# Performance work log

Hardware: AMD Instinct MI355X
Metric: run time of the kernel (lower is better)

Reference implementation:

```python
import jax, jax.numpy as jnp
import numpy as np

B, T, C, H = 4, 2048, 1024, 64


def setup_inputs() -> dict:
    key = jax.random.key(0)
    kx, kk, kq, kv = jax.random.split(key, 4)
    scale = 1.0 / np.sqrt(C)
    return {
        "x": jax.random.normal(kx, (B, T, C), dtype=jnp.float32),
        "Wk": jax.random.normal(kk, (C, H), dtype=jnp.float32) * scale,
        "Wq": jax.random.normal(kq, (C, H), dtype=jnp.float32) * scale,
        "Wv": jax.random.normal(kv, (C, H), dtype=jnp.float32) * scale,
    }


def reference(x, Wk, Wq, Wv):
    # projections: [B, T, H]
    k = jnp.einsum("btc,ch->bth", x, Wk)
    q = jnp.einsum("btc,ch->bth", x, Wq)
    v = jnp.einsum("btc,ch->bth", x, Wv)
    # attention scores [B, T, T], scaled by sqrt(head_size)
    scores = jnp.einsum("bqh,bkh->bqk", q, k) / jnp.sqrt(jnp.asarray(H, x.dtype))
    # causal mask (decoder)
    causal = jnp.tril(jnp.ones((T, T), dtype=bool))
    scores = jnp.where(causal, scores, -jnp.inf)
    attn = jax.nn.softmax(scores, axis=-1)
    # dropout p=0.0 (eval) -> identity
    return jnp.einsum("bqk,bkh->bqh", attn, v)
```

## Files before the change

### kernel.cpp

```cpp
#include <hip/hip_runtime.h>
#include <hip/hip_bf16.h>

#define BB 4
#define TT 2048
#define CC 1024
#define HH 64
#define LOG2E 1.4426950408889634f

typedef __attribute__((ext_vector_type(8))) unsigned short ushort8;
typedef __attribute__((ext_vector_type(4))) unsigned short ushort4v;
typedef __attribute__((ext_vector_type(8))) __bf16 bf16x8;
typedef __attribute__((ext_vector_type(4))) float float4v;

static __device__ __forceinline__ unsigned short f2bf(float f) {
    return __builtin_bit_cast(unsigned short, (__bf16)f);
}

static __device__ __forceinline__ float4v mfma16(ushort8 a, ushort8 b, float4v c) {
    return __builtin_amdgcn_mfma_f32_16x16x32_bf16(
        __builtin_bit_cast(bf16x8, a), __builtin_bit_cast(bf16x8, b), c, 0, 0, 0);
}

static __device__ __forceinline__ ushort8 cvt8(float4v a, float4v b) {
    ushort8 r;
#pragma unroll
    for (int i = 0; i < 4; ++i) { r[i] = f2bf(a[i]); r[4 + i] = f2bf(b[i]); }
    return r;
}

__global__ __launch_bounds__(256) void wconv_kernel(
    const float* __restrict__ Wq, const float* __restrict__ Wk,
    const float* __restrict__ Wv, unsigned short* __restrict__ wf)
{
    __shared__ __align__(16) float ws[3][64][64];
    const int kc = blockIdx.x;
    const int t = threadIdx.x;
    const int r = t >> 2, c4 = (t & 3) << 4;
    const float* Ws[3] = {Wq, Wk, Wv};
#pragma unroll
    for (int y = 0; y < 3; ++y) {
        const float* src = Ws[y] + (size_t)(kc * 64 + r) * HH + c4;
#pragma unroll
        for (int i = 0; i < 4; ++i)
            *(float4v*)&ws[y][r][c4 + 4 * i] = *(const float4v*)(src + 4 * i);
    }
    __syncthreads();
#pragma unroll
    for (int i = 0; i < 6; ++i) {
        const int U = t + 256 * i;
        const int lane = U & 63, qq = U >> 6;
        const int nt = qq % 12, ks = qq / 12;
        const int y = nt >> 2;
        const int col = 16 * (nt & 3) + (lane & 15);
        const int kl = ks * 32 + 8 * (lane >> 4);
        ushort8 p;
#pragma unroll
        for (int j = 0; j < 8; ++j) p[j] = f2bf(ws[y][kl + j][col]);
        *(ushort8*)&wf[((size_t)kc * 1536 + U) * 8] = p;
    }
}

__global__ __launch_bounds__(768) void proj_kernel(
    const float* __restrict__ x, const unsigned short* __restrict__ wf,
    unsigned short* __restrict__ qo, unsigned short* __restrict__ ko,
    unsigned short* __restrict__ vo)
{
    __shared__ __align__(16) unsigned short xa[2][2048];

    const int t0 = blockIdx.x << 5;
    const int tid = threadIdx.x;
    const int w = tid >> 6;
    const int lane = tid & 63;
    const int l15 = lane & 15, g = lane >> 4;

    ushort8 bw[16][2];
#pragma unroll
    for (int kc = 0; kc < 16; ++kc)
#pragma unroll
        for (int ks = 0; ks < 2; ++ks)
            bw[kc][ks] = *(const ushort8*)
                &wf[(size_t)(((kc * 2 + ks) * 12 + w) * 64 + lane) * 8];

    const int sr = tid >> 3, su = tid & 7;
    const int soff = (sr * 8 + (su ^ (sr & 7))) * 8;
    const float* xp = x + (size_t)(t0 + sr) * CC + su * 8;

    const int sw = l15 & 7;
    const int r00 = (l15 * 8 + (g ^ sw)) * 8;
    const int r01 = (l15 * 8 + ((4 + g) ^ sw)) * 8;
    const int r10 = ((16 + l15) * 8 + (g ^ sw)) * 8;
    const int r11 = ((16 + l15) * 8 + ((4 + g) ^ sw)) * 8;

    float4v ac0 = (float4v)0.0f, ac1 = (float4v)0.0f;

    if (tid < 256)
        *(ushort8*)&xa[0][soff] =
            cvt8(*(const float4v*)xp, *(const float4v*)(xp + 4));
    __syncthreads();

#pragma unroll
    for (int kc = 0; kc < 16; ++kc) {
        const int cur = kc & 1, nxt = cur ^ 1;
        float4v u0, u1;
        if (kc < 15 && tid < 256) {
            u0 = *(const float4v*)(xp + (kc + 1) * 64);
            u1 = *(const float4v*)(xp + (kc + 1) * 64 + 4);
        }
        const unsigned short* xb = xa[cur];
        ushort8 a00 = *(const ushort8*)&xb[r00];
        ushort8 a01 = *(const ushort8*)&xb[r01];
        ushort8 a10 = *(const ushort8*)&xb[r10];
        ushort8 a11 = *(const ushort8*)&xb[r11];
        if (w < 8) {
            ac0 = mfma16(a00, bw[kc][0], ac0);
            ac0 = mfma16(a01, bw[kc][1], ac0);
            ac1 = mfma16(a10, bw[kc][0], ac1);
            ac1 = mfma16(a11, bw[kc][1], ac1);
        } else {
            ac0 = mfma16(bw[kc][0], a00, ac0);
            ac0 = mfma16(bw[kc][1], a01, ac0);
            ac1 = mfma16(bw[kc][0], a10, ac1);
            ac1 = mfma16(bw[kc][1], a11, ac1);
        }
        if (kc < 15 && tid < 256)
            *(ushort8*)&xa[nxt][soff] = cvt8(u0, u1);
        __syncthreads();
    }

    if (w < 8) {
        const float sc = (w < 4) ? 0.125f * LOG2E : 1.0f;
        unsigned short* dst = (w < 4) ? qo : ko;
        const int nf = w & 3;
#pragma unroll
        for (int mt = 0; mt < 2; ++mt) {
            float4v a = mt ? ac1 : ac0;
#pragma unroll
            for (int r = 0; r < 4; ++r)
                dst[(size_t)(t0 + 16 * mt + 4 * g + r) * HH + 16 * nf + l15] =
                    f2bf(a[r] * sc);
        }
    } else {
        const int nf = w - 8;
        const int b = t0 >> 11, tl = t0 & (TT - 1);
#pragma unroll
        for (int mt = 0; mt < 2; ++mt) {
            float4v a = mt ? ac1 : ac0;
#pragma unroll
            for (int r = 0; r < 4; ++r)
                vo[((size_t)b * HH + 16 * nf + 4 * g + r) * TT + tl + 16 * mt + l15] =
                    f2bf(a[r]);
        }
    }
}

__global__ __launch_bounds__(512) void attn_kernel(
    const unsigned short* __restrict__ qw,
    const unsigned short* __restrict__ kw,
    const unsigned short* __restrict__ vw,
    float* __restrict__ out)
{
    __shared__ float om[8][16], ol[8][16];
    __shared__ __align__(16) float oo[8][16][64];

    const int idx = blockIdx.x;
    const int b = idx & (BB - 1);
    const int qt = (TT / 16 - 1) - (idx >> 2);
    const int q0 = qt << 4;
    const int tid = threadIdx.x;
    const int w = tid >> 6;
    const int lane = tid & 63;
    const int l15 = lane & 15;
    const int g = lane >> 4;
    const int q = q0 + l15;

    const unsigned short* qrow = qw + (size_t)(b * TT + q) * HH + 8 * g;
    ushort8 qf0 = *(const ushort8*)qrow;
    ushort8 qf1 = *(const ushort8*)(qrow + 32);

    const unsigned short* kb = kw + (size_t)b * TT * HH;
    const unsigned short* vb = vw + (size_t)b * HH * TT;

    float m_run = -3.0e38f, l_run = 0.0f;
    float4v o[4];
#pragma unroll
    for (int i = 0; i < 4; ++i) o[i] = (float4v)0.0f;

    for (int kv0 = 128 * w; kv0 < q0 + 16; kv0 += 1024) {
        const unsigned short* kr = kb + (size_t)(kv0 + l15) * HH + 8 * g;
        ushort8 akl[8], akh[8];
#pragma unroll
        for (int f = 0; f < 8; ++f) {
            akl[f] = *(const ushort8*)(kr + f * 16 * HH);
            akh[f] = *(const ushort8*)(kr + f * 16 * HH + 32);
        }
        ushort8 av[4][4];
#pragma unroll
        for (int ht = 0; ht < 4; ++ht) {
            const unsigned short* vp = vb + (size_t)(16 * ht + l15) * TT + kv0 + 4 * g;
#pragma unroll
            for (int g2 = 0; g2 < 4; ++g2) {
                ushort4v v0 = *(const ushort4v*)(vp + 32 * g2);
                ushort4v v1 = *(const ushort4v*)(vp + 32 * g2 + 16);
#pragma unroll
                for (int r = 0; r < 4; ++r) {
                    av[ht][g2][r] = v0[r]; av[ht][g2][4 + r] = v1[r];
                }
            }
        }

        float4v s[8];
#pragma unroll
        for (int f = 0; f < 8; ++f) {
            s[f] = mfma16(akl[f], qf0, (float4v)0.0f);
            s[f] = mfma16(akh[f], qf1, s[f]);
        }

        if (kv0 + 127 > q0) {
#pragma unroll
            for (int f = 0; f < 8; ++f)
#pragma unroll
                for (int r = 0; r < 4; ++r)
                    if (kv0 + 16 * f + 4 * g + r > q) s[f][r] = -1e30f;
        }

        float mt = s[0][0];
#pragma unroll
        for (int f = 0; f < 8; ++f)
#pragma unroll
            for (int r = 0; r < 4; ++r) mt = fmaxf(mt, s[f][r]);
        mt = fmaxf(mt, __shfl_xor(mt, 16, 64));
        mt = fmaxf(mt, __shfl_xor(mt, 32, 64));

        const float m_new = fmaxf(m_run, mt);
        const float scale = exp2f(m_run - m_new);
        float sum = 0.0f;
#pragma unroll
        for (int f = 0; f < 8; ++f)
#pragma unroll
            for (int r = 0; r < 4; ++r) {
                s[f][r] = exp2f(s[f][r] - m_new);
                sum += s[f][r];
            }
        sum += __shfl_xor(sum, 16, 64);
        sum += __shfl_xor(sum, 32, 64);
        l_run = l_run * scale + sum;
        m_run = m_new;
#pragma unroll
        for (int i = 0; i < 4; ++i) o[i] *= scale;

        ushort8 bp[4];
#pragma unroll
        for (int g2 = 0; g2 < 4; ++g2)
#pragma unroll
            for (int r = 0; r < 4; ++r) {
                bp[g2][r] = f2bf(s[2 * g2][r]);
                bp[g2][4 + r] = f2bf(s[2 * g2 + 1][r]);
            }
#pragma unroll
        for (int ht = 0; ht < 4; ++ht)
#pragma unroll
            for (int g2 = 0; g2 < 4; ++g2)
                o[ht] = mfma16(av[ht][g2], bp[g2], o[ht]);
    }

    if (lane < 16) { om[w][lane] = m_run; ol[w][lane] = l_run; }
#pragma unroll
    for (int ht = 0; ht < 4; ++ht)
        *(float4v*)&oo[w][l15][16 * ht + 4 * g] = o[ht];
    __syncthreads();

#pragma unroll 2
    for (int e = tid; e < 16 * HH; e += 512) {
        const int qq = e >> 6, h = e & 63;
        float mstar = om[0][qq];
#pragma unroll
        for (int w2 = 1; w2 < 8; ++w2) mstar = fmaxf(mstar, om[w2][qq]);
        float lsum = 0.0f, osum = 0.0f;
#pragma unroll
        for (int w2 = 0; w2 < 8; ++w2) {
            const float al = exp2f(om[w2][qq] - mstar);
            lsum += al * ol[w2][qq];
            osum += al * oo[w2][qq][h];
        }
        out[((size_t)b * TT + q0 + qq) * HH + h] = osum / lsum;
    }
}

extern "C" void kernel_launch(void* const* d_in, const int* in_sizes, int n_in,
                              void* d_out, int out_size, void* d_ws, size_t ws_size,
                              hipStream_t stream) {
    const float* x  = (const float*)d_in[0];
    const float* Wk = (const float*)d_in[1];
    const float* Wq = (const float*)d_in[2];
    const float* Wv = (const float*)d_in[3];

    unsigned short* q_ws  = (unsigned short*)d_ws;
    unsigned short* k_ws  = q_ws + (size_t)BB * TT * HH;
    unsigned short* vt_ws = k_ws + (size_t)BB * TT * HH;
    unsigned short* wf_ws = vt_ws + (size_t)BB * TT * HH;

    wconv_kernel<<<16, 256, 0, stream>>>(Wq, Wk, Wv, wf_ws);
    proj_kernel<<<BB * TT / 32, 768, 0, stream>>>(x, wf_ws, q_ws, k_ws, vt_ws);
    attn_kernel<<<BB * TT / 16, 512, 0, stream>>>(q_ws, k_ws, vt_ws, (float*)d_out);
}
```

Measured before the change: 53.04 us.

## Pipeline weight/x loads in projection, halve attention KV step, parallelize weight conversion

The weight-conversion kernel now runs on 96 blocks, using a transposed padded shared tile, and folds the Q scale into the weights. The projection kernel streams weight fragments with a two-step register prefetch and x rows four chunks ahead, instead of preloading all weights into registers. It also uses a lighter barrier. The attention kernel processes 64-key chunks per wave instead of 128, with launch bounds requesting two blocks per CU. Per-lane row-sum shuffles are deferred to the final merge via a per-group shared array. Together these aim to lower register pressure and raise occupancy and memory overlap, at the cost of more loop iterations and more complex indexing.

```diff
diff --git a/kernel.cpp b/kernel.cpp
--- a/kernel.cpp
+++ b/kernel.cpp
@@ -6,6 +6,7 @@
 #define CC 1024
 #define HH 64
 #define LOG2E 1.4426950408889634f
+#define QSCALE (0.125f * LOG2E)
 
 typedef __attribute__((ext_vector_type(8))) unsigned short ushort8;
 typedef __attribute__((ext_vector_type(4))) unsigned short ushort4v;
@@ -28,36 +29,39 @@
     return r;
 }
 
+#define BARRIER()                                            \
+    do {                                                     \
+        asm volatile("s_waitcnt lgkmcnt(0)" ::: "memory");   \
+        __builtin_amdgcn_s_barrier();                        \
+        asm volatile("" ::: "memory");                       \
+    } while (0)
+
 __global__ __launch_bounds__(256) void wconv_kernel(
     const float* __restrict__ Wq, const float* __restrict__ Wk,
     const float* __restrict__ Wv, unsigned short* __restrict__ wf)
 {
-    __shared__ __align__(16) float ws[3][64][64];
-    const int kc = blockIdx.x;
+    __shared__ __align__(16) float wsT[3][64][68];
+    const int kc = blockIdx.x / 6, part = blockIdx.x % 6;
     const int t = threadIdx.x;
-    const int r = t >> 2, c4 = (t & 3) << 4;
+    const int r = t >> 2, c0 = (t & 3) << 4;
     const float* Ws[3] = {Wq, Wk, Wv};
 #pragma unroll
     for (int y = 0; y < 3; ++y) {
-        const float* src = Ws[y] + (size_t)(kc * 64 + r) * HH + c4;
-#pragma unroll
-        for (int i = 0; i < 4; ++i)
-            *(float4v*)&ws[y][r][c4 + 4 * i] = *(const float4v*)(src + 4 * i);
+        const float* src = Ws[y] + (size_t)(kc * 64 + r) * HH + c0;
+        const float sc = (y == 0) ? QSCALE : 1.0f;
+#pragma unroll
+        for (int i = 0; i < 16; ++i) wsT[y][c0 + i][r] = src[i] * sc;
     }
     __syncthreads();
-#pragma unroll
-    for (int i = 0; i < 6; ++i) {
-        const int U = t + 256 * i;
-        const int lane = U & 63, qq = U >> 6;
-        const int nt = qq % 12, ks = qq / 12;
-        const int y = nt >> 2;
-        const int col = 16 * (nt & 3) + (lane & 15);
-        const int kl = ks * 32 + 8 * (lane >> 4);
-        ushort8 p;
-#pragma unroll
-        for (int j = 0; j < 8; ++j) p[j] = f2bf(ws[y][kl + j][col]);
-        *(ushort8*)&wf[((size_t)kc * 1536 + U) * 8] = p;
-    }
+    const int U = part * 256 + t;
+    const int lane = U & 63, qq = U >> 6;
+    const int nt = qq % 12, ks = qq / 12;
+    const int y = nt >> 2;
+    const int col = 16 * (nt & 3) + (lane & 15);
+    const int kl = ks * 32 + 8 * (lane >> 4);
+    float4v v0 = *(const float4v*)&wsT[y][col][kl];
+    float4v v1 = *(const float4v*)&wsT[y][col][kl + 4];
+    *(ushort8*)&wf[((size_t)kc * 1536 + U) * 8] = cvt8(v0, v1);
 }
 
 __global__ __launch_bounds__(768) void proj_kernel(
@@ -73,17 +77,28 @@
     const int lane = tid & 63;
     const int l15 = lane & 15, g = lane >> 4;
 
-    ushort8 bw[16][2];
-#pragma unroll
-    for (int kc = 0; kc < 16; ++kc)
-#pragma unroll
-        for (int ks = 0; ks < 2; ++ks)
-            bw[kc][ks] = *(const ushort8*)
-                &wf[(size_t)(((kc * 2 + ks) * 12 + w) * 64 + lane) * 8];
-
+    const bool stg = tid < 256;
     const int sr = tid >> 3, su = tid & 7;
     const int soff = (sr * 8 + (su ^ (sr & 7))) * 8;
     const float* xp = x + (size_t)(t0 + sr) * CC + su * 8;
+
+    float4v xr[4][2];
+    if (stg) {
+#pragma unroll
+        for (int p = 0; p < 4; ++p) {
+            xr[p][0] = *(const float4v*)(xp + p * 64);
+            xr[p][1] = *(const float4v*)(xp + p * 64 + 4);
+        }
+    }
+
+    const unsigned short* wfp = wf + ((size_t)w * 64 + lane) * 8;
+    ushort8 bc0 = *(const ushort8*)(wfp);
+    ushort8 bc1 = *(const ushort8*)(wfp + 6144);
+    ushort8 bn0 = *(const ushort8*)(wfp + 2 * 6144);
+    ushort8 bn1 = *(const ushort8*)(wfp + 3 * 6144);
+
+    if (stg) *(ushort8*)&xa[0][soff] = cvt8(xr[0][0], xr[0][1]);
+    BARRIER();
 
     const int sw = l15 & 7;
     const int r00 = (l15 * 8 + (g ^ sw)) * 8;
@@ -93,18 +108,17 @@
 
     float4v ac0 = (float4v)0.0f, ac1 = (float4v)0.0f;
 
-    if (tid < 256)
-        *(ushort8*)&xa[0][soff] =
-            cvt8(*(const float4v*)xp, *(const float4v*)(xp + 4));
-    __syncthreads();
-
 #pragma unroll
     for (int kc = 0; kc < 16; ++kc) {
-        const int cur = kc & 1, nxt = cur ^ 1;
-        float4v u0, u1;
-        if (kc < 15 && tid < 256) {
-            u0 = *(const float4v*)(xp + (kc + 1) * 64);
-            u1 = *(const float4v*)(xp + (kc + 1) * 64 + 4);
+        const int cur = kc & 1;
+        if (stg && kc + 4 < 16) {
+            xr[kc & 3][0] = *(const float4v*)(xp + (kc + 4) * 64);
+            xr[kc & 3][1] = *(const float4v*)(xp + (kc + 4) * 64 + 4);
+        }
+        ushort8 nw0, nw1;
+        if (kc + 2 < 16) {
+            nw0 = *(const ushort8*)(wfp + (size_t)(2 * kc + 4) * 6144);
+            nw1 = *(const ushort8*)(wfp + (size_t)(2 * kc + 5) * 6144);
         }
         const unsigned short* xb = xa[cur];
         ushort8 a00 = *(const ushort8*)&xb[r00];
@@ -112,23 +126,25 @@
         ushort8 a10 = *(const ushort8*)&xb[r10];
         ushort8 a11 = *(const ushort8*)&xb[r11];
         if (w < 8) {
-            ac0 = mfma16(a00, bw[kc][0], ac0);
-            ac0 = mfma16(a01, bw[kc][1], ac0);
-            ac1 = mfma16(a10, bw[kc][0], ac1);
-            ac1 = mfma16(a11, bw[kc][1], ac1);
+            ac0 = mfma16(a00, bc0, ac0);
+            ac0 = mfma16(a01, bc1, ac0);
+            ac1 = mfma16(a10, bc0, ac1);
+            ac1 = mfma16(a11, bc1, ac1);
         } else {
-            ac0 = mfma16(bw[kc][0], a00, ac0);
-            ac0 = mfma16(bw[kc][1], a01, ac0);
-            ac1 = mfma16(bw[kc][0], a10, ac1);
-            ac1 = mfma16(bw[kc][1], a11, ac1);
-        }
-        if (kc < 15 && tid < 256)
-            *(ushort8*)&xa[nxt][soff] = cvt8(u0, u1);
-        __syncthreads();
+            ac0 = mfma16(bc0, a00, ac0);
+            ac0 = mfma16(bc1, a01, ac0);
+            ac1 = mfma16(bc0, a10, ac1);
+            ac1 = mfma16(bc1, a11, ac1);
+        }
+        if (stg && kc + 1 < 16)
+            *(ushort8*)&xa[cur ^ 1][soff] =
+                cvt8(xr[(kc + 1) & 3][0], xr[(kc + 1) & 3][1]);
+        BARRIER();
+        bc0 = bn0; bc1 = bn1;
+        if (kc + 2 < 16) { bn0 = nw0; bn1 = nw1; }
     }
 
     if (w < 8) {
-        const float sc = (w < 4) ? 0.125f * LOG2E : 1.0f;
         unsigned short* dst = (w < 4) ? qo : ko;
         const int nf = w & 3;
 #pragma unroll
@@ -137,7 +153,7 @@
 #pragma unroll
             for (int r = 0; r < 4; ++r)
                 dst[(size_t)(t0 + 16 * mt + 4 * g + r) * HH + 16 * nf + l15] =
-                    f2bf(a[r] * sc);
+                    f2bf(a[r]);
         }
     } else {
         const int nf = w - 8;
@@ -153,13 +169,14 @@
     }
 }
 
-__global__ __launch_bounds__(512) void attn_kernel(
+__global__ __launch_bounds__(512, 2) void attn_kernel(
     const unsigned short* __restrict__ qw,
     const unsigned short* __restrict__ kw,
     const unsigned short* __restrict__ vw,
     float* __restrict__ out)
 {
-    __shared__ float om[8][16], ol[8][16];
+    __shared__ float om[8][16];
+    __shared__ float olg[8][4][16];
     __shared__ __align__(16) float oo[8][16][64];
 
     const int idx = blockIdx.x;
@@ -185,39 +202,40 @@
 #pragma unroll
     for (int i = 0; i < 4; ++i) o[i] = (float4v)0.0f;
 
-    for (int kv0 = 128 * w; kv0 < q0 + 16; kv0 += 1024) {
+    for (int kv0 = 64 * w; kv0 < q0 + 16; kv0 += 512) {
         const unsigned short* kr = kb + (size_t)(kv0 + l15) * HH + 8 * g;
-        ushort8 akl[8], akh[8];
-#pragma unroll
-        for (int f = 0; f < 8; ++f) {
+        ushort8 akl[4], akh[4];
+#pragma unroll
+        for (int f = 0; f < 4; ++f) {
             akl[f] = *(const ushort8*)(kr + f * 16 * HH);
             akh[f] = *(const ushort8*)(kr + f * 16 * HH + 32);
         }
-        ushort8 av[4][4];
+        ushort8 av[4][2];
 #pragma unroll
         for (int ht = 0; ht < 4; ++ht) {
             const unsigned short* vp = vb + (size_t)(16 * ht + l15) * TT + kv0 + 4 * g;
 #pragma unroll
-            for (int g2 = 0; g2 < 4; ++g2) {
+            for (int g2 = 0; g2 < 2; ++g2) {
                 ushort4v v0 = *(const ushort4v*)(vp + 32 * g2);
                 ushort4v v1 = *(const ushort4v*)(vp + 32 * g2 + 16);
 #pragma unroll
                 for (int r = 0; r < 4; ++r) {
-                    av[ht][g2][r] = v0[r]; av[ht][g2][4 + r] = v1[r];
+                    av[ht][g2][r] = v0[r];
+                    av[ht][g2][4 + r] = v1[r];
                 }
             }
         }
 
-        float4v s[8];
-#pragma unroll
-        for (int f = 0; f < 8; ++f) {
+        float4v s[4];
+#pragma unroll
+        for (int f = 0; f < 4; ++f) {
             s[f] = mfma16(akl[f], qf0, (float4v)0.0f);
             s[f] = mfma16(akh[f], qf1, s[f]);
         }
 
-        if (kv0 + 127 > q0) {
-#pragma unroll
-            for (int f = 0; f < 8; ++f)
+        if (kv0 + 63 > q0) {
+#pragma unroll
+            for (int f = 0; f < 4; ++f)
 #pragma unroll
                 for (int r = 0; r < 4; ++r)
                     if (kv0 + 16 * f + 4 * g + r > q) s[f][r] = -1e30f;
@@ -225,7 +243,7 @@
 
         float mt = s[0][0];
 #pragma unroll
-        for (int f = 0; f < 8; ++f)
+        for (int f = 0; f < 4; ++f)
 #pragma unroll
             for (int r = 0; r < 4; ++r) mt = fmaxf(mt, s[f][r]);
         mt = fmaxf(mt, __shfl_xor(mt, 16, 64));
@@ -235,35 +253,32 @@
         const float scale = exp2f(m_run - m_new);
         float sum = 0.0f;
 #pragma unroll
-        for (int f = 0; f < 8; ++f)
+        for (int f = 0; f < 4; ++f)
 #pragma unroll
             for (int r = 0; r < 4; ++r) {
                 s[f][r] = exp2f(s[f][r] - m_new);
                 sum += s[f][r];
             }
-        sum += __shfl_xor(sum, 16, 64);
-        sum += __shfl_xor(sum, 32, 64);
         l_run = l_run * scale + sum;
         m_run = m_new;
 #pragma unroll
         for (int i = 0; i < 4; ++i) o[i] *= scale;
 
-        ushort8 bp[4];
-#pragma unroll
-        for (int g2 = 0; g2 < 4; ++g2)
-#pragma unroll
-            for (int r = 0; r < 4; ++r) {
-                bp[g2][r] = f2bf(s[2 * g2][r]);
-                bp[g2][4 + r] = f2bf(s[2 * g2 + 1][r]);
-            }
-#pragma unroll
-        for (int ht = 0; ht < 4; ++ht)
-#pragma unroll
-            for (int g2 = 0; g2 < 4; ++g2)
-                o[ht] = mfma16(av[ht][g2], bp[g2], o[ht]);
-    }
-
-    if (lane < 16) { om[w][lane] = m_run; ol[w][lane] = l_run; }
+        ushort8 bp[2];
+#pragma unroll
+        for (int r = 0; r < 4; ++r) {
+            bp[0][r] = f2bf(s[0][r]); bp[0][4 + r] = f2bf(s[1][r]);
+            bp[1][r] = f2bf(s[2][r]); bp[1][4 + r] = f2bf(s[3][r]);
+        }
+#pragma unroll
+        for (int ht = 0; ht < 4; ++ht) {
+            o[ht] = mfma16(av[ht][0], bp[0], o[ht]);
+            o[ht] = mfma16(av[ht][1], bp[1], o[ht]);
+        }
+    }
+
+    if (lane < 16) om[w][lane] = m_run;
+    olg[w][g][l15] = l_run;
 #pragma unroll
     for (int ht = 0; ht < 4; ++ht)
         *(float4v*)&oo[w][l15][16 * ht + 4 * g] = o[ht];
@@ -279,7 +294,9 @@
 #pragma unroll
         for (int w2 = 0; w2 < 8; ++w2) {
             const float al = exp2f(om[w2][qq] - mstar);
-            lsum += al * ol[w2][qq];
+            const float lw = olg[w2][0][qq] + olg[w2][1][qq] +
+                             olg[w2][2][qq] + olg[w2][3][qq];
+            lsum += al * lw;
             osum += al * oo[w2][qq][h];
         }
         out[((size_t)b * TT + q0 + qq) * HH + h] = osum / lsum;
@@ -299,7 +316,7 @@
     unsigned short* vt_ws = k_ws + (size_t)BB * TT * HH;
     unsigned short* wf_ws = vt_ws + (size_t)BB * TT * HH;
 
-    wconv_kernel<<<16, 256, 0, stream>>>(Wq, Wk, Wv, wf_ws);
+    wconv_kernel<<<96, 256, 0, stream>>>(Wq, Wk, Wv, wf_ws);
     proj_kernel<<<BB * TT / 32, 768, 0, stream>>>(x, wf_ws, q_ws, k_ws, vt_ws);
     attn_kernel<<<BB * TT / 16, 512, 0, stream>>>(q_ws, k_ws, vt_ws, (float*)d_out);
 }
```

Result: slower. 55.13 us (+3.9%).
